# Kernel optimization log

Measured on AMD Instinct MI355X. Metric: run time of the kernel, lower is better.

The kernel has to match this reference:

```python
import jax, jax.numpy as jnp
import numpy as np

N_NODES = 50000
N_EDGES = 600000
HIDDEN = 128


def _sage_conv(x, src, dst, W_l, W_r, b):
    """PyG SAGEConv with mean aggregation:
    out_i = W_l @ mean_{j in N(i)} x_j + W_r @ x_i + b
    src/dst: [E] edge endpoints (message flows src -> dst).
    """
    msg = x[src]  # [E, d] gather
    agg = jax.ops.segment_sum(msg, dst, num_segments=N_NODES)  # [N, d]
    cnt = jax.ops.segment_sum(jnp.ones((src.shape[0],), x.dtype), dst,
                              num_segments=N_NODES)  # [N]
    mean = agg / jnp.maximum(cnt, 1.0)[:, None]
    return mean @ W_l.T + x @ W_r.T + b


def setup_inputs() -> dict:
    key = jax.random.key(0)
    ks = jax.random.split(key, 12)
    x = jax.random.normal(ks[0], (N_NODES, HIDDEN), dtype=jnp.float32)
    edge_index = jax.random.randint(ks[1], (2, N_EDGES), 0, N_NODES, dtype=jnp.int64)
    scale = 1.0 / np.sqrt(HIDDEN)
    inp = {"x": x, "edge_index": edge_index}
    for i, layer in enumerate(["1", "2", "3"]):
        inp["Wl" + layer] = jax.random.uniform(ks[2 + 3 * i], (HIDDEN, HIDDEN),
                                               minval=-scale, maxval=scale, dtype=jnp.float32)
        inp["Wr" + layer] = jax.random.uniform(ks[3 + 3 * i], (HIDDEN, HIDDEN),
                                               minval=-scale, maxval=scale, dtype=jnp.float32)
        inp["b" + layer] = jax.random.uniform(ks[4 + 3 * i], (HIDDEN,),
                                              minval=-scale, maxval=scale, dtype=jnp.float32)
    return inp


def reference(x, edge_index, Wl1, Wr1, b1, Wl2, Wr2, b2, Wl3, Wr3, b3):
    src, dst = edge_index[0], edge_index[1]
    h = jax.nn.relu(_sage_conv(x, src, dst, Wl1, Wr1, b1))
    h = _sage_conv(h, src, dst, Wl2, Wr2, b2)
    h = _sage_conv(h, src, dst, Wl3, Wr3, b3)
    return h
```

## Files before the change

### kernel.cpp

```cpp
#include <hip/hip_runtime.h>
#include <hip/hip_bf16.h>

#define N_NODES 50000
#define N_EDGES 600000
#define HID 128

typedef __attribute__((ext_vector_type(8))) short s8v;
typedef __attribute__((ext_vector_type(8))) unsigned short u8v;
typedef __attribute__((ext_vector_type(4))) float f4v;

__device__ __forceinline__ unsigned short f2bf(float x) {
    unsigned u = __float_as_uint(x);
    unsigned r = u + 0x7FFFu + ((u >> 16) & 1u);
    return (unsigned short)(r >> 16);
}
__device__ __forceinline__ float bf2f(unsigned short u) {
    return __uint_as_float((unsigned)u << 16);
}
__device__ __forceinline__ void split_bf(float x, unsigned short& hi, unsigned short& lo) {
    hi = f2bf(x);
    lo = f2bf(x - bf2f(hi));
}

__device__ __forceinline__ int detect_m64(const void* edges) {
    const int* p = (const int*)edges;
    int lane = threadIdx.x & 63;
    unsigned long long nz = __ballot(p[2 * lane + 1] != 0);
    return (nz == 0ULL) ? 1 : 0;
}

__device__ __forceinline__ int edge_at(const void* edges, int mode64, long long idx) {
    return mode64 ? (int)((const long long*)edges)[idx] : ((const int*)edges)[idx];
}

__global__ __launch_bounds__(256) void prep(
    const void* __restrict__ edges, const float* __restrict__ x,
    const float* __restrict__ m0, const float* __restrict__ m1,
    const float* __restrict__ m2, const float* __restrict__ m3,
    const float* __restrict__ m4, const float* __restrict__ m5,
    int* __restrict__ deg, int* __restrict__ rank,
    unsigned short* __restrict__ whi, unsigned short* __restrict__ wlo,
    unsigned short* __restrict__ xhi, unsigned short* __restrict__ xlo) {
    const int EB  = (N_EDGES + 255) / 256;
    const int WCV = (6 * HID * HID + 255) / 256;
    const int b = blockIdx.x;
    if (b < EB) {
        int m = detect_m64(edges);
        int e = b * 256 + threadIdx.x;
        if (e >= N_EDGES) return;
        int d = edge_at(edges, m, (long long)N_EDGES + e);
        if ((unsigned)d < (unsigned)N_NODES)
            rank[e] = atomicAdd(&deg[d], 1);
    } else if (b < EB + WCV) {
        int idx = (b - EB) * 256 + threadIdx.x;
        if (idx >= 6 * HID * HID) return;
        int mat = idx >> 14, off = idx & 16383;
        const float* src = mat == 0 ? m0 : mat == 1 ? m1 : mat == 2 ? m2
                         : mat == 3 ? m3 : mat == 4 ? m4 : m5;
        unsigned short h, l;
        split_bf(src[off], h, l);
        whi[idx] = h; wlo[idx] = l;
    } else {
        const int n4 = (N_NODES * HID) / 4;
        int i = (b - EB - WCV) * 256 + threadIdx.x;
        if (i >= n4) return;
        float4 v = ((const float4*)x)[i];
        ushort4 h, l;
        split_bf(v.x, h.x, l.x);
        split_bf(v.y, h.y, l.y);
        split_bf(v.z, h.z, l.z);
        split_bf(v.w, h.w, l.w);
        ((ushort4*)xhi)[i] = h;
        ((ushort4*)xlo)[i] = l;
    }
}

__global__ void scan_block(const int* __restrict__ deg, int* __restrict__ offs,
                           int* __restrict__ blocksum) {
    __shared__ int sm[256];
    int i = blockIdx.x * 256 + threadIdx.x;
    int v = (i < N_NODES) ? deg[i] : 0;
    sm[threadIdx.x] = v;
    __syncthreads();
    #pragma unroll
    for (int s = 1; s < 256; s <<= 1) {
        int t = (threadIdx.x >= (unsigned)s) ? sm[threadIdx.x - s] : 0;
        __syncthreads();
        sm[threadIdx.x] += t;
        __syncthreads();
    }
    if (i < N_NODES) offs[i] = sm[threadIdx.x] - v;
    if (threadIdx.x == 255) blocksum[blockIdx.x] = sm[255];
}

__global__ void scan_add(int* __restrict__ offs,
                         const int* __restrict__ blocksum, int nblocks) {
    __shared__ int sm[256];
    int t = threadIdx.x;
    int bv = (t < nblocks) ? blocksum[t] : 0;
    sm[t] = (t < (int)blockIdx.x) ? bv : 0;
    __syncthreads();
    #pragma unroll
    for (int s = 128; s > 0; s >>= 1) {
        if (t < s) sm[t] += sm[t + s];
        __syncthreads();
    }
    int prefix = sm[0];
    int i = blockIdx.x * 256 + t;
    if (i < N_NODES) offs[i] += prefix;
    if ((int)blockIdx.x == nblocks - 1 && t == 0)
        offs[N_NODES] = prefix + blocksum[nblocks - 1];
}

__global__ void fill_csr(const void* __restrict__ edges, const int* __restrict__ rank,
                         const int* __restrict__ offs, int* __restrict__ csr) {
    int m = detect_m64(edges);
    int e = blockIdx.x * 256 + threadIdx.x;
    if (e >= N_EDGES) return;
    int d = edge_at(edges, m, (long long)N_EDGES + e);
    int s = edge_at(edges, m, (long long)e);
    if ((unsigned)d >= (unsigned)N_NODES || (unsigned)s >= (unsigned)N_NODES) return;
    csr[offs[d] + rank[e]] = s;
}

__global__ __launch_bounds__(256) void aggregate_bf16(const unsigned short* __restrict__ h,
                                                      const int* __restrict__ offs,
                                                      const int* __restrict__ csr,
                                                      unsigned short* __restrict__ mhi,
                                                      unsigned short* __restrict__ mlo) {
    const int sub  = threadIdx.x & 15;
    const int node = blockIdx.x * 16 + (threadIdx.x >> 4);
    if (node >= N_NODES) return;
    const int beg = offs[node], end = offs[node + 1];
    float a[8] = {0.f, 0.f, 0.f, 0.f, 0.f, 0.f, 0.f, 0.f};
    int p = beg;
    for (; p + 8 <= end; p += 8) {
        int s0 = csr[p],     s1 = csr[p + 1], s2 = csr[p + 2], s3 = csr[p + 3];
        int s4 = csr[p + 4], s5 = csr[p + 5], s6 = csr[p + 6], s7 = csr[p + 7];
        u8v v0 = *(const u8v*)(h + (size_t)s0 * HID + sub * 8);
        u8v v1 = *(const u8v*)(h + (size_t)s1 * HID + sub * 8);
        u8v v2 = *(const u8v*)(h + (size_t)s2 * HID + sub * 8);
        u8v v3 = *(const u8v*)(h + (size_t)s3 * HID + sub * 8);
        u8v v4 = *(const u8v*)(h + (size_t)s4 * HID + sub * 8);
        u8v v5 = *(const u8v*)(h + (size_t)s5 * HID + sub * 8);
        u8v v6 = *(const u8v*)(h + (size_t)s6 * HID + sub * 8);
        u8v v7 = *(const u8v*)(h + (size_t)s7 * HID + sub * 8);
        #pragma unroll
        for (int j = 0; j < 8; ++j)
            a[j] += ((bf2f(v0[j]) + bf2f(v1[j])) + (bf2f(v2[j]) + bf2f(v3[j])))
                  + ((bf2f(v4[j]) + bf2f(v5[j])) + (bf2f(v6[j]) + bf2f(v7[j])));
    }
    if (p + 4 <= end) {
        int s0 = csr[p], s1 = csr[p + 1], s2 = csr[p + 2], s3 = csr[p + 3];
        u8v v0 = *(const u8v*)(h + (size_t)s0 * HID + sub * 8);
        u8v v1 = *(const u8v*)(h + (size_t)s1 * HID + sub * 8);
        u8v v2 = *(const u8v*)(h + (size_t)s2 * HID + sub * 8);
        u8v v3 = *(const u8v*)(h + (size_t)s3 * HID + sub * 8);
        #pragma unroll
        for (int j = 0; j < 8; ++j)
            a[j] += (bf2f(v0[j]) + bf2f(v1[j])) + (bf2f(v2[j]) + bf2f(v3[j]));
        p += 4;
    }
    for (; p < end; ++p) {
        int s = csr[p];
        u8v v = *(const u8v*)(h + (size_t)s * HID + sub * 8);
        #pragma unroll
        for (int j = 0; j < 8; ++j) a[j] += bf2f(v[j]);
    }
    const float inv = 1.0f / fmaxf((float)(end - beg), 1.0f);
    u8v hh, ll;
    #pragma unroll
    for (int j = 0; j < 8; ++j) {
        unsigned short hj, lj;
        split_bf(a[j] * inv, hj, lj);
        hh[j] = hj; ll[j] = lj;
    }
    *(u8v*)(mhi + (size_t)node * HID + sub * 8) = hh;
    *(u8v*)(mlo + (size_t)node * HID + sub * 8) = ll;
}

template <int RELU, int FINAL>
__global__ __launch_bounds__(256) void sage_mfma(
    const unsigned short* __restrict__ Mhi, const unsigned short* __restrict__ Mlo,
    const unsigned short* __restrict__ Hhi, const unsigned short* __restrict__ Hlo,
    const unsigned short* __restrict__ Whi, const unsigned short* __restrict__ Wlo,
    const float* __restrict__ bias,
    unsigned short* __restrict__ ohi, unsigned short* __restrict__ olo,
    float* __restrict__ of32) {
    __shared__ short BhS[128 * 72];
    __shared__ short BlS[128 * 72];
    const int tid = threadIdx.x;
    const int wave = tid >> 6, lane = tid & 63;
    const int mIdx = lane & 15, q = lane >> 4;
    const int wrow = (wave & 1) * 64, wcol = (wave >> 1) * 64;
    const int rowBase = blockIdx.x * 128;

    size_t aoff[4];
    #pragma unroll
    for (int t = 0; t < 4; ++t) {
        int node = rowBase + wrow + t * 16 + mIdx;
        if (node > N_NODES - 1) node = N_NODES - 1;
        aoff[t] = (size_t)node * HID + q * 8;
    }

    const int bcol = tid & 127;
    const int bseg = (tid >> 7) * 32;

    f4v acc[4][4];
    #pragma unroll
    for (int a = 0; a < 4; ++a)
        #pragma unroll
        for (int b = 0; b < 4; ++b) acc[a][b] = (f4v){0.f, 0.f, 0.f, 0.f};

    s8v Ah[2][4], Al[2][4];
    auto loadA = [&](int i, int buf) {
        const unsigned short* ah_ = (i < 4) ? Mhi : Hhi;
        const unsigned short* al_ = (i < 4) ? Mlo : Hlo;
        const int kc = (i & 3) * 32;
        #pragma unroll
        for (int t = 0; t < 4; ++t) {
            Ah[buf][t] = *(const s8v*)(ah_ + aoff[t] + kc);
            Al[buf][t] = *(const s8v*)(al_ + aoff[t] + kc);
        }
    };

    loadA(0, 0);
    for (int panel = 0; panel < 4; ++panel) {
        const int ph = panel >> 1;
        const int kb = (panel & 1) * 64;
        const unsigned short* Wh_ = Whi + ph * HID * HID;
        const unsigned short* Wl_ = Wlo + ph * HID * HID;
        __syncthreads();
        {
            const unsigned short* sh = Wh_ + bcol * HID + kb + bseg;
            const unsigned short* sl = Wl_ + bcol * HID + kb + bseg;
            short* dh = BhS + bcol * 72 + bseg;
            short* dl = BlS + bcol * 72 + bseg;
            #pragma unroll
            for (int j = 0; j < 4; ++j) {
                *(s8v*)(dh + j * 8) = *(const s8v*)(sh + j * 8);
                *(s8v*)(dl + j * 8) = *(const s8v*)(sl + j * 8);
            }
        }
        __syncthreads();
        #pragma unroll
        for (int c = 0; c < 2; ++c) {
            const int i = panel * 2 + c;
            if (i < 7) loadA(i + 1, (i + 1) & 1);
            const int kc2 = c * 32;
            s8v Bh_f[4], Bl_f[4];
            #pragma unroll
            for (int nt = 0; nt < 4; ++nt) {
                const int a = (wcol + nt * 16 + mIdx) * 72 + kc2 + q * 8;
                Bh_f[nt] = *(const s8v*)(BhS + a);
                Bl_f[nt] = *(const s8v*)(BlS + a);
            }
            const int buf = i & 1;
            #pragma unroll
            for (int mt = 0; mt < 4; ++mt)
                #pragma unroll
                for (int nt = 0; nt < 4; ++nt) {
                    acc[mt][nt] = __builtin_amdgcn_mfma_f32_16x16x32_bf16(
                        Ah[buf][mt], Bh_f[nt], acc[mt][nt], 0, 0, 0);
                    acc[mt][nt] = __builtin_amdgcn_mfma_f32_16x16x32_bf16(
                        Al[buf][mt], Bh_f[nt], acc[mt][nt], 0, 0, 0);
                    acc[mt][nt] = __builtin_amdgcn_mfma_f32_16x16x32_bf16(
                        Ah[buf][mt], Bl_f[nt], acc[mt][nt], 0, 0, 0);
                }
        }
    }

    float bv[4];
    #pragma unroll
    for (int nt = 0; nt < 4; ++nt) bv[nt] = bias[wcol + nt * 16 + mIdx];

    #pragma unroll
    for (int mt = 0; mt < 4; ++mt)
        #pragma unroll
        for (int r = 0; r < 4; ++r) {
            int node = rowBase + wrow + mt * 16 + q * 4 + r;
            if (node < N_NODES) {
                #pragma unroll
                for (int nt = 0; nt < 4; ++nt) {
                    int feat = wcol + nt * 16 + mIdx;
                    float v = acc[mt][nt][r] + bv[nt];
                    if (RELU) v = fmaxf(v, 0.f);
                    size_t oidx = (size_t)node * HID + feat;
                    if (FINAL) {
                        of32[oidx] = v;
                    } else {
                        unsigned short hh, ll;
                        split_bf(v, hh, ll);
                        ohi[oidx] = hh;
                        olo[oidx] = ll;
                    }
                }
            }
        }
}

extern "C" void kernel_launch(void* const* d_in, const int* in_sizes, int n_in,
                              void* d_out, int out_size, void* d_ws, size_t ws_size,
                              hipStream_t stream) {
    const float* x   = (const float*)d_in[0];
    const void* edges = d_in[1];
    const float* Wl1 = (const float*)d_in[2];
    const float* Wr1 = (const float*)d_in[3];
    const float* b1  = (const float*)d_in[4];
    const float* Wl2 = (const float*)d_in[5];
    const float* Wr2 = (const float*)d_in[6];
    const float* b2  = (const float*)d_in[7];
    const float* Wl3 = (const float*)d_in[8];
    const float* Wr3 = (const float*)d_in[9];
    const float* b3  = (const float*)d_in[10];
    float* out = (float*)d_out;

    char* ws = (char*)d_ws;
    size_t off = 0;
    auto alloc = [&](size_t bytes) -> void* {
        void* p = (void*)(ws + off);
        off += (bytes + 255) & ~(size_t)255;
        return p;
    };
    typedef unsigned short u16;
    const size_t FEAT = (size_t)N_NODES * HID;
    int* deg      = (int*)alloc((size_t)N_NODES * 4);
    int* rank     = (int*)alloc((size_t)N_EDGES * 4);
    int* offs     = (int*)alloc((size_t)(N_NODES + 1) * 4);
    int* blocksum = (int*)alloc(256 * 4);
    int* csr      = (int*)alloc((size_t)N_EDGES * 4);
    u16* whi      = (u16*)alloc((size_t)6 * HID * HID * 2);
    u16* wlo      = (u16*)alloc((size_t)6 * HID * HID * 2);
    u16* xhi      = (u16*)alloc(FEAT * 2);
    u16* xlo      = (u16*)alloc(FEAT * 2);
    u16* h1hi     = (u16*)alloc(FEAT * 2);
    u16* h1lo     = (u16*)alloc(FEAT * 2);
    u16* mhi      = (u16*)alloc(FEAT * 2);
    u16* mlo      = (u16*)alloc(FEAT * 2);
    (void)ws_size; (void)in_sizes; (void)n_in; (void)out_size;

    const int EB    = (N_EDGES + 255) / 256;
    const int NB    = (N_NODES + 255) / 256;
    const int WCV   = (6 * HID * HID + 255) / 256;
    const int XSP   = ((int)(FEAT / 4) + 255) / 256;
    const int PREPB = EB + WCV + XSP;
    const int AGG_B = (N_NODES + 15) / 16;
    const int GEMM_B = (N_NODES + 127) / 128;

    hipMemsetAsync(deg, 0, (size_t)N_NODES * 4, stream);
    prep<<<PREPB, 256, 0, stream>>>(edges, x, Wl1, Wr1, Wl2, Wr2, Wl3, Wr3,
                                    deg, rank, whi, wlo, xhi, xlo);
    scan_block<<<NB, 256, 0, stream>>>(deg, offs, blocksum);
    scan_add<<<NB, 256, 0, stream>>>(offs, blocksum, NB);
    fill_csr<<<EB, 256, 0, stream>>>(edges, rank, offs, csr);

    aggregate_bf16<<<AGG_B, 256, 0, stream>>>(xhi, offs, csr, mhi, mlo);
    sage_mfma<1, 0><<<GEMM_B, 256, 0, stream>>>(mhi, mlo, xhi, xlo,
        whi, wlo, b1, h1hi, h1lo, (float*)nullptr);
    aggregate_bf16<<<AGG_B, 256, 0, stream>>>(h1hi, offs, csr, mhi, mlo);
    sage_mfma<0, 0><<<GEMM_B, 256, 0, stream>>>(mhi, mlo, h1hi, h1lo,
        whi + 2 * HID * HID, wlo + 2 * HID * HID, b2, xhi, xlo, (float*)nullptr);
    aggregate_bf16<<<AGG_B, 256, 0, stream>>>(xhi, offs, csr, mhi, mlo);
    sage_mfma<0, 1><<<GEMM_B, 256, 0, stream>>>(mhi, mlo, xhi, xlo,
        whi + 4 * HID * HID, wlo + 4 * HID * HID, b3,
        (u16*)nullptr, (u16*)nullptr, out);
}
```

Measured before the change: 308.4 us.

## Fuse CSR scan and fill into cooperative kernel; halve GEMM row tile

```diff
diff --git a/kernel.cpp b/kernel.cpp
--- a/kernel.cpp
+++ b/kernel.cpp
@@ -1,5 +1,8 @@
 #include <hip/hip_runtime.h>
 #include <hip/hip_bf16.h>
+#include <hip/hip_cooperative_groups.h>
+
+namespace cg = cooperative_groups;
 
 #define N_NODES 50000
 #define N_EDGES 600000
@@ -75,52 +78,57 @@
     }
 }
 
-__global__ void scan_block(const int* __restrict__ deg, int* __restrict__ offs,
-                           int* __restrict__ blocksum) {
+__global__ __launch_bounds__(256) void csr_build(
+    const void* __restrict__ edges, const int* __restrict__ rank,
+    const int* __restrict__ deg, int* __restrict__ offs,
+    int* __restrict__ blocksum, int* __restrict__ csr) {
+    cg::grid_group grid = cg::this_grid();
     __shared__ int sm[256];
-    int i = blockIdx.x * 256 + threadIdx.x;
-    int v = (i < N_NODES) ? deg[i] : 0;
-    sm[threadIdx.x] = v;
-    __syncthreads();
-    #pragma unroll
-    for (int s = 1; s < 256; s <<= 1) {
-        int t = (threadIdx.x >= (unsigned)s) ? sm[threadIdx.x - s] : 0;
+    const int NB = (N_NODES + 255) / 256;
+    const int t = threadIdx.x;
+
+    if ((int)blockIdx.x < NB) {
+        int i = blockIdx.x * 256 + t;
+        int v = (i < N_NODES) ? deg[i] : 0;
+        sm[t] = v;
         __syncthreads();
-        sm[threadIdx.x] += t;
+        #pragma unroll
+        for (int s = 1; s < 256; s <<= 1) {
+            int u = (t >= s) ? sm[t - s] : 0;
+            __syncthreads();
+            sm[t] += u;
+            __syncthreads();
+        }
+        if (i < N_NODES) offs[i] = sm[t] - v;
+        if (t == 255) blocksum[blockIdx.x] = sm[255];
+    }
+    grid.sync();
+    if ((int)blockIdx.x < NB) {
+        int bv = (t < NB) ? blocksum[t] : 0;
+        sm[t] = (t < (int)blockIdx.x) ? bv : 0;
         __syncthreads();
-    }
-    if (i < N_NODES) offs[i] = sm[threadIdx.x] - v;
-    if (threadIdx.x == 255) blocksum[blockIdx.x] = sm[255];
-}
-
-__global__ void scan_add(int* __restrict__ offs,
-                         const int* __restrict__ blocksum, int nblocks) {
-    __shared__ int sm[256];
-    int t = threadIdx.x;
-    int bv = (t < nblocks) ? blocksum[t] : 0;
-    sm[t] = (t < (int)blockIdx.x) ? bv : 0;
-    __syncthreads();
-    #pragma unroll
-    for (int s = 128; s > 0; s >>= 1) {
-        if (t < s) sm[t] += sm[t + s];
-        __syncthreads();
-    }
-    int prefix = sm[0];
-    int i = blockIdx.x * 256 + t;
-    if (i < N_NODES) offs[i] += prefix;
-    if ((int)blockIdx.x == nblocks - 1 && t == 0)
-        offs[N_NODES] = prefix + blocksum[nblocks - 1];
-}
-
-__global__ void fill_csr(const void* __restrict__ edges, const int* __restrict__ rank,
-                         const int* __restrict__ offs, int* __restrict__ csr) {
-    int m = detect_m64(edges);
-    int e = blockIdx.x * 256 + threadIdx.x;
-    if (e >= N_EDGES) return;
-    int d = edge_at(edges, m, (long long)N_EDGES + e);
-    int s = edge_at(edges, m, (long long)e);
-    if ((unsigned)d >= (unsigned)N_NODES || (unsigned)s >= (unsigned)N_NODES) return;
-    csr[offs[d] + rank[e]] = s;
+        #pragma unroll
+        for (int s = 128; s > 0; s >>= 1) {
+            if (t < s) sm[t] += sm[t + s];
+            __syncthreads();
+        }
+        int prefix = sm[0];
+        int i = blockIdx.x * 256 + t;
+        if (i < N_NODES) offs[i] += prefix;
+        if ((int)blockIdx.x == NB - 1 && t == 0)
+            offs[N_NODES] = prefix + blocksum[NB - 1];
+    }
+    grid.sync();
+    const int m = detect_m64(edges);
+    const int EB = (N_EDGES + 255) / 256;
+    for (int lb = blockIdx.x; lb < EB; lb += gridDim.x) {
+        int e = lb * 256 + t;
+        if (e >= N_EDGES) continue;
+        int d = edge_at(edges, m, (long long)N_EDGES + e);
+        int s = edge_at(edges, m, (long long)e);
+        if ((unsigned)d >= (unsigned)N_NODES || (unsigned)s >= (unsigned)N_NODES) continue;
+        csr[offs[d] + rank[e]] = s;
+    }
 }
 
 __global__ __launch_bounds__(256) void aggregate_bf16(const unsigned short* __restrict__ h,
@@ -180,7 +188,7 @@
 }
 
 template <int RELU, int FINAL>
-__global__ __launch_bounds__(256) void sage_mfma(
+__global__ __launch_bounds__(256, 4) void sage_mfma(
     const unsigned short* __restrict__ Mhi, const unsigned short* __restrict__ Mlo,
     const unsigned short* __restrict__ Hhi, const unsigned short* __restrict__ Hlo,
     const unsigned short* __restrict__ Whi, const unsigned short* __restrict__ Wlo,
@@ -192,12 +200,12 @@
     const int tid = threadIdx.x;
     const int wave = tid >> 6, lane = tid & 63;
     const int mIdx = lane & 15, q = lane >> 4;
-    const int wrow = (wave & 1) * 64, wcol = (wave >> 1) * 64;
-    const int rowBase = blockIdx.x * 128;
-
-    size_t aoff[4];
-    #pragma unroll
-    for (int t = 0; t < 4; ++t) {
+    const int wrow = (wave & 1) * 32, wcol = (wave >> 1) * 64;
+    const int rowBase = blockIdx.x * 64;
+
+    size_t aoff[2];
+    #pragma unroll
+    for (int t = 0; t < 2; ++t) {
         int node = rowBase + wrow + t * 16 + mIdx;
         if (node > N_NODES - 1) node = N_NODES - 1;
         aoff[t] = (size_t)node * HID + q * 8;
@@ -206,19 +214,19 @@
     const int bcol = tid & 127;
     const int bseg = (tid >> 7) * 32;
 
-    f4v acc[4][4];
-    #pragma unroll
-    for (int a = 0; a < 4; ++a)
+    f4v acc[2][4];
+    #pragma unroll
+    for (int a = 0; a < 2; ++a)
         #pragma unroll
         for (int b = 0; b < 4; ++b) acc[a][b] = (f4v){0.f, 0.f, 0.f, 0.f};
 
-    s8v Ah[2][4], Al[2][4];
+    s8v Ah[2][2], Al[2][2];
     auto loadA = [&](int i, int buf) {
         const unsigned short* ah_ = (i < 4) ? Mhi : Hhi;
         const unsigned short* al_ = (i < 4) ? Mlo : Hlo;
         const int kc = (i & 3) * 32;
         #pragma unroll
-        for (int t = 0; t < 4; ++t) {
+        for (int t = 0; t < 2; ++t) {
             Ah[buf][t] = *(const s8v*)(ah_ + aoff[t] + kc);
             Al[buf][t] = *(const s8v*)(al_ + aoff[t] + kc);
         }
@@ -257,7 +265,7 @@
             }
             const int buf = i & 1;
             #pragma unroll
-            for (int mt = 0; mt < 4; ++mt)
+            for (int mt = 0; mt < 2; ++mt)
                 #pragma unroll
                 for (int nt = 0; nt < 4; ++nt) {
                     acc[mt][nt] = __builtin_amdgcn_mfma_f32_16x16x32_bf16(
@@ -275,7 +283,7 @@
     for (int nt = 0; nt < 4; ++nt) bv[nt] = bias[wcol + nt * 16 + mIdx];
 
     #pragma unroll
-    for (int mt = 0; mt < 4; ++mt)
+    for (int mt = 0; mt < 2; ++mt)
         #pragma unroll
         for (int r = 0; r < 4; ++r) {
             int node = rowBase + wrow + mt * 16 + q * 4 + r;
@@ -340,19 +348,21 @@
     (void)ws_size; (void)in_sizes; (void)n_in; (void)out_size;
 
     const int EB    = (N_EDGES + 255) / 256;
-    const int NB    = (N_NODES + 255) / 256;
     const int WCV   = (6 * HID * HID + 255) / 256;
     const int XSP   = ((int)(FEAT / 4) + 255) / 256;
     const int PREPB = EB + WCV + XSP;
     const int AGG_B = (N_NODES + 15) / 16;
-    const int GEMM_B = (N_NODES + 127) / 128;
+    const int GEMM_B = (N_NODES + 63) / 64;
 
     hipMemsetAsync(deg, 0, (size_t)N_NODES * 4, stream);
     prep<<<PREPB, 256, 0, stream>>>(edges, x, Wl1, Wr1, Wl2, Wr2, Wl3, Wr3,
                                     deg, rank, whi, wlo, xhi, xlo);
-    scan_block<<<NB, 256, 0, stream>>>(deg, offs, blocksum);
-    scan_add<<<NB, 256, 0, stream>>>(offs, blocksum, NB);
-    fill_csr<<<EB, 256, 0, stream>>>(edges, rank, offs, csr);
+    {
+        void* args[] = { (void*)&edges, (void*)&rank, (void*)&deg,
+                         (void*)&offs, (void*)&blocksum, (void*)&csr };
+        hipLaunchCooperativeKernel((const void*)csr_build, dim3(1024), dim3(256),
+                                   args, 0, stream);
+    }
 
     aggregate_bf16<<<AGG_B, 256, 0, stream>>>(xhi, offs, csr, mhi, mlo);
     sage_mfma<1, 0><<<GEMM_B, 256, 0, stream>>>(mhi, mlo, xhi, xlo,
```

New measurement: 571.8 us. 1.85x slower.
